# Kernel optimization log

Measured on AMD Instinct MI355X. Metric: run time of the kernel, lower is better.

Reference implementation:

```python
import jax, jax.numpy as jnp
import numpy as np

B = 4096
D = 64  # emb_dim, hardcoded in UserEmb/ItemEmb


def setup_inputs() -> dict:
    key = jax.random.key(0)
    ks = jax.random.split(key, 26)
    n = lambda k, shape, s=1.0: jax.random.normal(k, shape, dtype=jnp.float32) * s
    inp = {
        'user_emb': jax.random.randint(ks[0], (B, 4), 0, 6, dtype=jnp.int32),
        'item_emb': jax.random.randint(ks[1], (B, 10242), 0, 2, dtype=jnp.int32),
        'edge_emb': jnp.zeros((B,), dtype=jnp.int32),  # edges_emb has num_embeddings=1
        # UserEmb params
        'gender_tab': n(ks[2], (98, D)),
        'age_tab': n(ks[3], (7, D)),
        'occ_tab': n(ks[4], (21, D)),
        'area_tab': n(ks[5], (3402, D)),
        'user_W': n(ks[6], (4 * D, D), 0.05),  # stored [in,out]
        'user_b': n(ks[7], (D,), 0.05),
        # ItemEmb params
        'rate_tab': n(ks[8], (6, D)),
        'genre_W': n(ks[9], (25, D), 0.05),
        'director_W': n(ks[10], (2186, D), 0.02),
        'actor_W': n(ks[11], (8030, D), 0.01),
        'item_W': n(ks[12], (4 * D, D), 0.05),
        'item_b': n(ks[13], (D,), 0.05),
        # GLNFeat params (torch: randn * 0.5)
        'edges_tab': n(ks[14], (1, D)),
        'uu_w': n(ks[15], (D,), 0.5),
        'ui_w': n(ks[16], (D,), 0.5),
        'iu_w': n(ks[17], (D,), 0.5),
        'ii_w': n(ks[18], (D,), 0.5),
        'edge_W': n(ks[19], (D, D), 0.5),
        'uu_W1': n(ks[20], (D, D), 0.5),
        'ui_W1': n(ks[21], (D, D), 0.5),
        'iu_W1': n(ks[22], (D, D), 0.5),
        'ii_W1': n(ks[23], (D, D), 0.5),
    }
    return inp


def _lrelu(v):
    return jnp.where(v >= 0, v, 0.01 * v)  # nn.LeakyReLU default slope


def reference(user_emb, item_emb, edge_emb, gender_tab, age_tab, occ_tab, area_tab,
              user_W, user_b, rate_tab, genre_W, director_W, actor_W, item_W, item_b,
              edges_tab, uu_w, ui_w, iu_w, ii_w, edge_W, uu_W1, ui_W1, iu_W1, ii_W1):
    a = 0.12
    b = 0.12
    # UserEmb
    u_cat = jnp.concatenate([gender_tab[user_emb[:, 0]], age_tab[user_emb[:, 1]],
                             occ_tab[user_emb[:, 2]], area_tab[user_emb[:, 3]]], axis=1)
    x = (u_cat @ user_W + user_b) * a  # [B, D]
    # ItemEmb: multi-hot fields projected then mean-normalized by count
    genre = item_emb[:, 1:26].astype(jnp.float32)
    director = item_emb[:, 26:2212].astype(jnp.float32)
    actor = item_emb[:, 2212:10242].astype(jnp.float32)
    ge = (genre @ genre_W) / jnp.sum(genre, 1, keepdims=True)
    de = (director @ director_W) / jnp.sum(director, 1, keepdims=True)
    ae = (actor @ actor_W) / jnp.sum(actor, 1, keepdims=True)
    i_cat = jnp.concatenate([rate_tab[item_emb[:, 0]], ge, de, ae], axis=1)
    y = (i_cat @ item_W + item_b) * a  # [B, D]
    edge = edges_tab[edge_emb] * b  # [B, D]

    def outer_mm(u, v, M):
        # stop_gradient(outer(u, v) @ M) == u[:,None] * (v @ M), avoids [B,B]
        return jax.lax.stop_gradient(u[:, None] * (v @ M))

    xe = x * edge
    ye = y * edge
    x_xx = xe @ uu_w      # [B]
    x_xy_x = xe @ ui_w
    x_xy_y = ye @ ui_w
    t1 = outer_mm(x_xx, x_xx, x)
    t2 = outer_mm(x_xy_x, x_xy_y, y)
    x_buy = (_lrelu(t1 @ uu_W1) + _lrelu(t2 @ ui_W1)) / 2
    y_yy = ye @ ii_w
    y_yx_y = ye @ iu_w
    y_yx_x = xe @ iu_w
    t3 = outer_mm(y_yy, y_yy, y)
    t4 = outer_mm(y_yx_y, y_yx_x, x)
    y_buy = (_lrelu(t3 @ ii_W1) + _lrelu(t4 @ iu_W1)) / 2
    new = _lrelu(edge @ edge_W)
    return ((x_buy + x) / 2, (y_buy + y) / 2, (new + edge) / 2)
```

## Files before the change

kernel.cpp:

```cpp
#include <hip/hip_runtime.h>
#include <cstddef>

constexpr int BATCH = 4096;
constexpr int ITEM_COLS = 10242;

constexpr int R_GENDER = 0;
constexpr int R_AGE    = 98;
constexpr int R_OCC    = 105;
constexpr int R_AREA   = 126;
constexpr int R_RATE   = 3528;
constexpr int R_FU     = 3534;

__device__ const int CBASE[9]  = {0, 24, 1112, 2208, 3544, 4880, 6224, 7560, 8896};
__device__ const int VSTART[9] = {1, 26, 1119, 2212, 3550, 4888, 6227, 7565, 8903};
__device__ const int VEND[9]   = {26, 1119, 2212, 3550, 4888, 6227, 7565, 8903, 10242};
__device__ const int CUM[10]   = {0, 128, 1280, 2432, 3840, 5248, 6656, 8064, 9472, 10880};
constexpr int FB2COLS = 10880;
constexpr int NFUSEA = 884;
constexpr int NFUSET = FB2COLS / 64;

constexpr size_t OFF_FU  = 0;
constexpr size_t OFF_NEW = OFF_FU + (size_t)R_FU * 64;
constexpr size_t OFF_FBT = OFF_NEW + 64;
constexpr size_t OFF_X   = OFF_FBT + (size_t)64 * FB2COLS / 2;
constexpr size_t OFF_Y   = OFF_X + (size_t)BATCH * 64;
constexpr size_t OFF_P   = OFF_Y + (size_t)BATCH * 64;
constexpr size_t OFF_C   = OFF_P + 9ull * BATCH * 64;
constexpr size_t OFF_SP  = OFF_C + 9ull * BATCH;
constexpr size_t OFF_PB  = OFF_SP + 256ull * 256;
constexpr size_t OFF_SC  = OFF_PB + 4ull * 64;

typedef __attribute__((ext_vector_type(8))) short bf16x8;
typedef __attribute__((ext_vector_type(4))) float f32x4;

__device__ __forceinline__ float lrelu(float v) { return v >= 0.0f ? v : 0.01f * v; }

__device__ __forceinline__ unsigned bf_rne_pair(float lo, float hi) {
    unsigned ul = __builtin_bit_cast(unsigned, lo);
    unsigned uh = __builtin_bit_cast(unsigned, hi);
    ul += 0x7fffu + ((ul >> 16) & 1u);
    uh += 0x7fffu + ((uh >> 16) & 1u);
    return (ul >> 16) | (uh & 0xffff0000u);
}

__global__ __launch_bounds__(256) void k_fuse(
        const float* __restrict__ gender_tab, const float* __restrict__ age_tab,
        const float* __restrict__ occ_tab, const float* __restrict__ area_tab,
        const float* __restrict__ user_W, const float* __restrict__ rate_tab,
        const float* __restrict__ item_W, const float* __restrict__ edges_tab,
        const float* __restrict__ edge_W, const float* __restrict__ genre_W,
        const float* __restrict__ director_W, const float* __restrict__ actor_W,
        float* __restrict__ Fu, float* __restrict__ NEWt, short* __restrict__ Fbt2) {
    const int t = threadIdx.x;
    const int n = t & 63;
    const int rb = __builtin_amdgcn_readfirstlane(t >> 6);
    __shared__ float T[64 * 65];
    const int blk = blockIdx.x;

    if (blk < NFUSEA) {
        int r = blk * 4 + rb;
        if (r > R_FU) return;
        if (r == R_FU) {
            float acc = 0.0f;
#pragma unroll
            for (int k = 0; k < 64; ++k)
                acc = fmaf(edges_tab[k] * 0.12f, edge_W[k * 64 + n], acc);
            NEWt[n] = lrelu(acc);
            return;
        }
        const float* src;
        const float* W;
        if (r < R_AGE)       { src = gender_tab + (size_t)r * 64;            W = user_W;            }
        else if (r < R_OCC)  { src = age_tab    + (size_t)(r - R_AGE) * 64;  W = user_W + 64 * 64;  }
        else if (r < R_AREA) { src = occ_tab    + (size_t)(r - R_OCC) * 64;  W = user_W + 128 * 64; }
        else if (r < R_RATE) { src = area_tab   + (size_t)(r - R_AREA) * 64; W = user_W + 192 * 64; }
        else                 { src = rate_tab   + (size_t)(r - R_RATE) * 64; W = item_W;            }
        float acc = 0.0f;
#pragma unroll
        for (int k = 0; k < 64; ++k)
            acc = fmaf(src[k], W[k * 64 + n], acc);
        Fu[(size_t)r * 64 + n] = acc;
        return;
    }

    const int g0 = (blk - NFUSEA) * 64;
    int ch = 0;
    while (g0 >= CUM[ch + 1]) ++ch;
    const int kk0 = g0 - CUM[ch];
    const int lenp = CUM[ch + 1] - CUM[ch];
    const int cb = CBASE[ch], vs = VSTART[ch], ve = VEND[ch];

    for (int rl = 0; rl < 16; ++rl) {
        int r = rl * 4 + rb;
        int c = cb + kk0 + r;
        float acc = 0.0f;
        if (c >= vs && c < ve) {
            const float* src;
            const float* W;
            if (c < 26)        { src = genre_W    + (size_t)(c - 1) * 64;    W = item_W + 64 * 64;  }
            else if (c < 2212) { src = director_W + (size_t)(c - 26) * 64;   W = item_W + 128 * 64; }
            else               { src = actor_W    + (size_t)(c - 2212) * 64; W = item_W + 192 * 64; }
#pragma unroll
            for (int k = 0; k < 64; ++k)
                acc = fmaf(src[k], W[k * 64 + n], acc);
        }
        T[r * 65 + n] = acc;
    }
    __syncthreads();
    int n2 = t >> 2, sg = t & 3;
    unsigned dw[8];
#pragma unroll
    for (int d = 0; d < 8; ++d)
        dw[d] = bf_rne_pair(T[(sg * 16 + 2 * d) * 65 + n2], T[(sg * 16 + 2 * d + 1) * 65 + n2]);
    uint4* dst = (uint4*)(Fbt2 + (size_t)64 * CUM[ch] + (size_t)n2 * lenp + kk0 + sg * 16);
    dst[0] = make_uint4(dw[0], dw[1], dw[2], dw[3]);
    dst[1] = make_uint4(dw[4], dw[5], dw[6], dw[7]);
}

__global__ __launch_bounds__(256) void k_item(const int* __restrict__ item,
                                              const short* __restrict__ Fbt2,
                                              float* __restrict__ P, float* __restrict__ C) {
    const int ch = blockIdx.y;
    const int cb = CBASE[ch], vs = VSTART[ch], ve = VEND[ch];
    const int lo = vs - cb;
    const int hi = ve - cb;
    const int lenp = CUM[ch + 1] - CUM[ch];
    const short* FB = Fbt2 + (size_t)64 * CUM[ch];
    const int m0 = blockIdx.x * 64;
    const int t = threadIdx.x;
    const int lane = t & 63;
    const int w = __builtin_amdgcn_readfirstlane(t >> 6);
    const int q = lane >> 4, r16 = lane & 15;

    __shared__ short As[64 * 136];
    __shared__ short Bs[64 * 136];

    f32x4 acc[5];
#pragma unroll
    for (int s = 0; s < 5; ++s) acc[s] = (f32x4){0.f, 0.f, 0.f, 0.f};

    const short o = (r16 == 0) ? (short)0x3f80 : (short)0;
    const bf16x8 ones = {o, o, o, o, o, o, o, o};

    for (int kb = 0; kb < hi; kb += 128) {
        __syncthreads();
        const int c0 = cb + kb;
        if (c0 + 128 <= ITEM_COLS) {
#pragma unroll
            for (int it = 0; it < 16; ++it) {
                int f = it * 256 + t;
                int r = f >> 6, c2 = f & 63;
                int2 v = *(const int2*)(item + (size_t)(m0 + r) * ITEM_COLS + c0 + c2 * 2);
                unsigned d = (v.x ? 0x3f80u : 0u) | (v.y ? 0x3f800000u : 0u);
                *(unsigned*)(As + r * 136 + c2 * 2) = d;
            }
        } else {
#pragma unroll
            for (int it = 0; it < 32; ++it) {
                int f = it * 256 + t;
                int r = f >> 7, cc = f & 127;
                int c = c0 + cc;
                int v = (c < ITEM_COLS) ? item[(size_t)(m0 + r) * ITEM_COLS + c] : 0;
                As[r * 136 + cc] = v ? (short)0x3f80 : (short)0;
            }
        }
        {
            int nB = t >> 2, pt = t & 3;
            const short* fb = FB + (size_t)nB * lenp + kb;
#pragma unroll
            for (int p = 0; p < 4; ++p) {
                int off = (p * 4 + pt) * 8;
                *(uint4*)(Bs + nB * 136 + off) = *(const uint4*)(fb + off);
            }
        }
        __syncthreads();
        const bool edge = (kb < lo) || (kb + 128 > hi);
#pragma unroll
        for (int kt = 0; kt < 4; ++kt) {
            bf16x8 a = *(const bf16x8*)(As + (w * 16 + r16) * 136 + kt * 32 + q * 8);
            bf16x8 ov = ones;
            if (edge) {
#pragma unroll
                for (int j = 0; j < 8; ++j) {
                    int ks = kb + kt * 32 + q * 8 + j;
                    ov[j] = (ks >= lo && ks < hi) ? o : (short)0;
                }
            }
#pragma unroll
            for (int s = 0; s < 4; ++s) {
                bf16x8 b = *(const bf16x8*)(Bs + (s * 16 + r16) * 136 + kt * 32 + q * 8);
                acc[s] = __builtin_amdgcn_mfma_f32_16x16x32_bf16(a, b, acc[s], 0, 0, 0);
            }
            acc[4] = __builtin_amdgcn_mfma_f32_16x16x32_bf16(a, ov, acc[4], 0, 0, 0);
        }
    }
    const size_t pb = (size_t)ch * BATCH + m0 + w * 16 + q * 4;
#pragma unroll
    for (int reg = 0; reg < 4; ++reg) {
        float* pr = P + (pb + reg) * 64 + r16;
        pr[0] = acc[0][reg];
        pr[16] = acc[1][reg];
        pr[32] = acc[2][reg];
        pr[48] = acc[3][reg];
    }
    if (r16 == 0) {
#pragma unroll
        for (int reg = 0; reg < 4; ++reg)
            C[(size_t)ch * BATCH + m0 + w * 16 + q * 4 + reg] = acc[4][reg];
    }
}

__device__ __forceinline__ float wred(float v) {
#pragma unroll
    for (int m = 1; m < 64; m <<= 1) v += __shfl_xor(v, m, 64);
    return v;
}

__global__ __launch_bounds__(256) void k_mid(const int* __restrict__ item, const int* __restrict__ edge_emb,
                                             const int* __restrict__ user_emb,
                                             const float* __restrict__ Fu, const float* __restrict__ user_b,
                                             const float* __restrict__ P, const float* __restrict__ C,
                                             const float* __restrict__ item_b, const float* __restrict__ edges_tab,
                                             const float* __restrict__ uu_w, const float* __restrict__ ui_w,
                                             const float* __restrict__ iu_w, const float* __restrict__ ii_w,
                                             float* __restrict__ X, float* __restrict__ Y,
                                             float* __restrict__ SC, float* __restrict__ SP) {
    const int t = threadIdx.x;
    const int n = t & 63;
    const int wv = __builtin_amdgcn_readfirstlane(t >> 6);
    const float uuw = uu_w[n], uiw = ui_w[n], iuw = iu_w[n], iiw = ii_w[n];
    const float ib = item_b[n], ub = user_b[n];
    const size_t cs = (size_t)BATCH * 64;
    float s1 = 0.0f, s2 = 0.0f, s3 = 0.0f, s4 = 0.0f;

    for (int i = 0; i < 4; ++i) {
        int b = blockIdx.x * 16 + wv * 4 + i;
        const int* ue = user_emb + (size_t)b * 4;
        float x = (Fu[(size_t)(R_GENDER + ue[0]) * 64 + n]
                 + Fu[(size_t)(R_AGE    + ue[1]) * 64 + n]
                 + Fu[(size_t)(R_OCC    + ue[2]) * 64 + n]
                 + Fu[(size_t)(R_AREA   + ue[3]) * 64 + n] + ub) * 0.12f;
        X[(size_t)b * 64 + n] = x;
        int ri = item[(size_t)b * ITEM_COLS];
        size_t base = (size_t)b * 64 + n;
        float sg = P[base];
        float sd = P[base + cs] + P[base + 2 * cs];
        float sa = P[base + 3 * cs] + P[base + 4 * cs] + P[base + 5 * cs]
                 + P[base + 6 * cs] + P[base + 7 * cs] + P[base + 8 * cs];
        float cg = C[b];
        float cd = C[BATCH + b] + C[2 * BATCH + b];
        float ca = C[3 * BATCH + b] + C[4 * BATCH + b] + C[5 * BATCH + b]
                 + C[6 * BATCH + b] + C[7 * BATCH + b] + C[8 * BATCH + b];
        float y = (Fu[(size_t)(R_RATE + ri) * 64 + n] + sg / cg + sd / cd + sa / ca + ib) * 0.12f;
        Y[(size_t)b * 64 + n] = y;
        float e = edges_tab[(size_t)edge_emb[b] * 64 + n] * 0.12f;
        float xe = x * e, ye = y * e;
        float r1 = wred(xe * uuw);
        float r2 = wred(xe * uiw);
        float r3 = wred(xe * iuw);
        float r4 = wred(ye * uiw);
        float r5 = wred(ye * iiw);
        float r6 = wred(ye * iuw);
        if (n == 0) {
            SC[b] = r1; SC[BATCH + b] = r2; SC[2 * BATCH + b] = r5; SC[3 * BATCH + b] = r6;
        }
        s1 = fmaf(r1, x, s1);
        s2 = fmaf(r4, y, s2);
        s3 = fmaf(r5, y, s3);
        s4 = fmaf(r3, x, s4);
    }
    __shared__ float sp[4][4][64];
    sp[wv][0][n] = s1; sp[wv][1][n] = s2; sp[wv][2][n] = s3; sp[wv][3][n] = s4;
    __syncthreads();
    int i2 = t >> 6;
    float v = sp[0][i2][n] + sp[1][i2][n] + sp[2][i2][n] + sp[3][i2][n];
    SP[(size_t)blockIdx.x * 256 + t] = v;
}

__global__ __launch_bounds__(1024) void k_red(const float* __restrict__ SP,
                                              const float* __restrict__ uu_W1, const float* __restrict__ ui_W1,
                                              const float* __restrict__ iu_W1, const float* __restrict__ ii_W1,
                                              float* __restrict__ PB) {
    int t = threadIdx.x;
    int sub = t >> 8, i = (t >> 6) & 3, n = t & 63;
    float s = 0.0f;
    for (int wb = sub * 64; wb < sub * 64 + 64; ++wb)
        s += SP[(size_t)wb * 256 + i * 64 + n];
    __shared__ float red[4][4][64];
    red[sub][i][n] = s;
    __syncthreads();
    float sv = red[0][i][n] + red[1][i][n] + red[2][i][n] + red[3][i][n];
    __shared__ float sl[4][64];
    if (t < 256) sl[i][n] = sv;
    __syncthreads();
    if (t < 256) {
        const float* W1 = (i == 0) ? uu_W1 : (i == 1) ? ui_W1 : (i == 2) ? ii_W1 : iu_W1;
        float p = 0.0f;
#pragma unroll
        for (int k = 0; k < 64; ++k) p = fmaf(sl[i][k], W1[k * 64 + n], p);
        PB[i * 64 + n] = p;
    }
}

__global__ __launch_bounds__(256) void k_out(const float* __restrict__ X, const float* __restrict__ Y,
                                             const float* __restrict__ SC, const float* __restrict__ PB,
                                             const float* __restrict__ NEWt, const float* __restrict__ edges_tab,
                                             const int* __restrict__ edge_emb, float* __restrict__ out) {
    int t = threadIdx.x;
    int b = blockIdx.x * 4 + (t >> 6);
    int n = t & 63;
    float xx = SC[b], xyx = SC[BATCH + b], yy = SC[2 * BATCH + b], yxy = SC[3 * BATCH + b];
    float p1 = PB[n], p2 = PB[64 + n], p3 = PB[128 + n], p4 = PB[192 + n];
    float x = X[(size_t)b * 64 + n], y = Y[(size_t)b * 64 + n];
    float o1 = ((lrelu(xx * p1) + lrelu(xyx * p2)) * 0.5f + x) * 0.5f;
    float o2 = ((lrelu(yy * p3) + lrelu(yxy * p4)) * 0.5f + y) * 0.5f;
    int ei = edge_emb[b];
    float e = edges_tab[(size_t)ei * 64 + n] * 0.12f;
    float o3 = (NEWt[n] + e) * 0.5f;
    out[(size_t)b * 64 + n] = o1;
    out[((size_t)BATCH + b) * 64 + n] = o2;
    out[((size_t)2 * BATCH + b) * 64 + n] = o3;
}

extern "C" void kernel_launch(void* const* d_in, const int* in_sizes, int n_in,
                              void* d_out, int out_size, void* d_ws, size_t ws_size,
                              hipStream_t stream) {
    (void)in_sizes; (void)n_in; (void)out_size; (void)ws_size;
    const int*   user_emb   = (const int*)  d_in[0];
    const int*   item_emb   = (const int*)  d_in[1];
    const int*   edge_emb   = (const int*)  d_in[2];
    const float* gender_tab = (const float*)d_in[3];
    const float* age_tab    = (const float*)d_in[4];
    const float* occ_tab    = (const float*)d_in[5];
    const float* area_tab   = (const float*)d_in[6];
    const float* user_W     = (const float*)d_in[7];
    const float* user_b     = (const float*)d_in[8];
    const float* rate_tab   = (const float*)d_in[9];
    const float* genre_W    = (const float*)d_in[10];
    const float* director_W = (const float*)d_in[11];
    const float* actor_W    = (const float*)d_in[12];
    const float* item_W     = (const float*)d_in[13];
    const float* item_b     = (const float*)d_in[14];
    const float* edges_tab  = (const float*)d_in[15];
    const float* uu_w       = (const float*)d_in[16];
    const float* ui_w       = (const float*)d_in[17];
    const float* iu_w       = (const float*)d_in[18];
    const float* ii_w       = (const float*)d_in[19];
    const float* edge_W     = (const float*)d_in[20];
    const float* uu_W1      = (const float*)d_in[21];
    const float* ui_W1      = (const float*)d_in[22];
    const float* iu_W1      = (const float*)d_in[23];
    const float* ii_W1      = (const float*)d_in[24];

    float* ws   = (float*)d_ws;
    float* Fu   = ws + OFF_FU;
    float* NEWt = ws + OFF_NEW;
    short* Fbt2 = (short*)(ws + OFF_FBT);
    float* X    = ws + OFF_X;
    float* Y    = ws + OFF_Y;
    float* P    = ws + OFF_P;
    float* C    = ws + OFF_C;
    float* SP   = ws + OFF_SP;
    float* PB   = ws + OFF_PB;
    float* SC   = ws + OFF_SC;
    float* out  = (float*)d_out;

    hipLaunchKernelGGL(k_fuse, dim3(NFUSEA + NFUSET), dim3(256), 0, stream,
                       gender_tab, age_tab, occ_tab, area_tab, user_W, rate_tab,
                       item_W, edges_tab, edge_W, genre_W, director_W, actor_W,
                       Fu, NEWt, Fbt2);
    hipLaunchKernelGGL(k_item, dim3(BATCH / 64, 9), dim3(256), 0, stream, item_emb, Fbt2, P, C);
    hipLaunchKernelGGL(k_mid, dim3(BATCH / 16), dim3(256), 0, stream,
                       item_emb, edge_emb, user_emb, Fu, user_b, P, C, item_b, edges_tab,
                       uu_w, ui_w, iu_w, ii_w, X, Y, SC, SP);
    hipLaunchKernelGGL(k_red, dim3(1), dim3(1024), 0, stream, SP, uu_W1, ui_W1, iu_W1, ii_W1, PB);
    hipLaunchKernelGGL(k_out, dim3(BATCH / 4), dim3(256), 0, stream,
                       X, Y, SC, PB, NEWt, edges_tab, edge_emb, out);
}
```

Baseline: 348.8 us.

## Balance item GEMM k-slices, prefetch tiles into registers, fuse reduction into output

The item multi-hot GEMM is repartitioned from 9 uneven channel blocks into 15 balanced k-slices over a flat k-tile index. Each k-tile's A and B data is prefetched into registers while the current tile is consumed, with hand-placed barriers replacing __syncthreads. This aims to fix load imbalance and hide global load latency. The single-block k_red kernel is folded into k_out, so every output block redundantly reduces SP and computes the W1 projections. That removes one launch but adds duplicated reduction work per block.

```diff
diff --git a/kernel.cpp b/kernel.cpp
--- a/kernel.cpp
+++ b/kernel.cpp
@@ -11,11 +11,24 @@
 constexpr int R_RATE   = 3528;
 constexpr int R_FU     = 3534;
 
-__device__ const int CBASE[9]  = {0, 24, 1112, 2208, 3544, 4880, 6224, 7560, 8896};
-__device__ const int VSTART[9] = {1, 26, 1119, 2212, 3550, 4888, 6227, 7565, 8903};
-__device__ const int VEND[9]   = {26, 1119, 2212, 3550, 4888, 6227, 7565, 8903, 10242};
-__device__ const int CUM[10]   = {0, 128, 1280, 2432, 3840, 5248, 6656, 8064, 9472, 10880};
+__device__ const int CUM[10] = {0, 128, 1280, 2432, 3840, 5248, 6656, 8064, 9472, 10880};
+__device__ const int DLT[9]  = {0, -104, -168, -224, -296, -368, -432, -504, -576};
+__device__ const int LOG[9]  = {1, 130, 1287, 2436, 3846, 5256, 6659, 8069, 9479};
+__device__ const int HIG[9]  = {26, 1223, 2380, 3774, 5184, 6595, 7997, 9407, 10818};
 constexpr int FB2COLS = 10880;
+constexpr int NSLICE  = 15;
+__device__ const int TS_[16] = {0, 1, 7, 13, 19, 25, 31, 37, 43, 49, 55, 61, 67, 73, 79, 85};
+__device__ const int TCH[85] = {
+    0,
+    1,1,1,1,1,1,1,1,1,
+    2,2,2,2,2,2,2,2,2,
+    3,3,3,3,3,3,3,3,3,3,3,
+    4,4,4,4,4,4,4,4,4,4,4,
+    5,5,5,5,5,5,5,5,5,5,5,
+    6,6,6,6,6,6,6,6,6,6,6,
+    7,7,7,7,7,7,7,7,7,7,7,
+    8,8,8,8,8,8,8,8,8,8,8};
+
 constexpr int NFUSEA = 884;
 constexpr int NFUSET = FB2COLS / 64;
 
@@ -25,10 +38,9 @@
 constexpr size_t OFF_X   = OFF_FBT + (size_t)64 * FB2COLS / 2;
 constexpr size_t OFF_Y   = OFF_X + (size_t)BATCH * 64;
 constexpr size_t OFF_P   = OFF_Y + (size_t)BATCH * 64;
-constexpr size_t OFF_C   = OFF_P + 9ull * BATCH * 64;
-constexpr size_t OFF_SP  = OFF_C + 9ull * BATCH;
-constexpr size_t OFF_PB  = OFF_SP + 256ull * 256;
-constexpr size_t OFF_SC  = OFF_PB + 4ull * 64;
+constexpr size_t OFF_C   = OFF_P + (size_t)NSLICE * BATCH * 64;
+constexpr size_t OFF_SP  = OFF_C + (size_t)NSLICE * BATCH;
+constexpr size_t OFF_SC  = OFF_SP + 256ull * 256;
 
 typedef __attribute__((ext_vector_type(8))) short bf16x8;
 typedef __attribute__((ext_vector_type(4))) float f32x4;
@@ -86,15 +98,14 @@
     const int g0 = (blk - NFUSEA) * 64;
     int ch = 0;
     while (g0 >= CUM[ch + 1]) ++ch;
-    const int kk0 = g0 - CUM[ch];
-    const int lenp = CUM[ch + 1] - CUM[ch];
-    const int cb = CBASE[ch], vs = VSTART[ch], ve = VEND[ch];
+    const int lo = LOG[ch], hi = HIG[ch], dl = DLT[ch];
 
     for (int rl = 0; rl < 16; ++rl) {
         int r = rl * 4 + rb;
-        int c = cb + kk0 + r;
+        int g = g0 + r;
         float acc = 0.0f;
-        if (c >= vs && c < ve) {
+        if (g >= lo && g < hi) {
+            int c = g + dl;
             const float* src;
             const float* W;
             if (c < 26)        { src = genre_W    + (size_t)(c - 1) * 64;    W = item_W + 64 * 64;  }
@@ -112,7 +123,7 @@
 #pragma unroll
     for (int d = 0; d < 8; ++d)
         dw[d] = bf_rne_pair(T[(sg * 16 + 2 * d) * 65 + n2], T[(sg * 16 + 2 * d + 1) * 65 + n2]);
-    uint4* dst = (uint4*)(Fbt2 + (size_t)64 * CUM[ch] + (size_t)n2 * lenp + kk0 + sg * 16);
+    uint4* dst = (uint4*)(Fbt2 + (size_t)n2 * FB2COLS + g0 + sg * 16);
     dst[0] = make_uint4(dw[0], dw[1], dw[2], dw[3]);
     dst[1] = make_uint4(dw[4], dw[5], dw[6], dw[7]);
 }
@@ -120,12 +131,8 @@
 __global__ __launch_bounds__(256) void k_item(const int* __restrict__ item,
                                               const short* __restrict__ Fbt2,
                                               float* __restrict__ P, float* __restrict__ C) {
-    const int ch = blockIdx.y;
-    const int cb = CBASE[ch], vs = VSTART[ch], ve = VEND[ch];
-    const int lo = vs - cb;
-    const int hi = ve - cb;
-    const int lenp = CUM[ch + 1] - CUM[ch];
-    const short* FB = Fbt2 + (size_t)64 * CUM[ch];
+    const int slc = blockIdx.y;
+    const int kt0 = TS_[slc], kt1 = TS_[slc + 1];
     const int m0 = blockIdx.x * 64;
     const int t = threadIdx.x;
     const int lane = t & 63;
@@ -142,59 +149,75 @@
     const short o = (r16 == 0) ? (short)0x3f80 : (short)0;
     const bf16x8 ones = {o, o, o, o, o, o, o, o};
 
-    for (int kb = 0; kb < hi; kb += 128) {
-        __syncthreads();
-        const int c0 = cb + kb;
+    int2 av[16];
+    uint4 bv[4];
+    const int nB = t >> 2, pt = t & 3;
+    const int* arow = item + (size_t)(m0 + w) * ITEM_COLS + 2 * lane;
+    const short* brow = Fbt2 + (size_t)nB * FB2COLS;
+
+    auto fetch = [&](int kt) {
+        const int ch = TCH[kt];
+        const int c0 = kt * 128 + DLT[ch];
         if (c0 + 128 <= ITEM_COLS) {
+            const int* ap = arow + c0;
+#pragma unroll
+            for (int it = 0; it < 16; ++it)
+                av[it] = *(const int2*)(ap + (size_t)it * 4 * ITEM_COLS);
+        } else {
+            const bool ok = (c0 + 2 * lane) <= (ITEM_COLS - 2);
+            const int ccl = ok ? (c0 + 2 * lane) : (ITEM_COLS - 2);
+            const int* ap = item + (size_t)(m0 + w) * ITEM_COLS + ccl;
 #pragma unroll
             for (int it = 0; it < 16; ++it) {
-                int f = it * 256 + t;
-                int r = f >> 6, c2 = f & 63;
-                int2 v = *(const int2*)(item + (size_t)(m0 + r) * ITEM_COLS + c0 + c2 * 2);
-                unsigned d = (v.x ? 0x3f80u : 0u) | (v.y ? 0x3f800000u : 0u);
-                *(unsigned*)(As + r * 136 + c2 * 2) = d;
+                int2 v = *(const int2*)(ap + (size_t)it * 4 * ITEM_COLS);
+                av[it].x = ok ? v.x : 0;
+                av[it].y = ok ? v.y : 0;
             }
-        } else {
-#pragma unroll
-            for (int it = 0; it < 32; ++it) {
-                int f = it * 256 + t;
-                int r = f >> 7, cc = f & 127;
-                int c = c0 + cc;
-                int v = (c < ITEM_COLS) ? item[(size_t)(m0 + r) * ITEM_COLS + c] : 0;
-                As[r * 136 + cc] = v ? (short)0x3f80 : (short)0;
-            }
-        }
-        {
-            int nB = t >> 2, pt = t & 3;
-            const short* fb = FB + (size_t)nB * lenp + kb;
-#pragma unroll
-            for (int p = 0; p < 4; ++p) {
-                int off = (p * 4 + pt) * 8;
-                *(uint4*)(Bs + nB * 136 + off) = *(const uint4*)(fb + off);
-            }
-        }
-        __syncthreads();
-        const bool edge = (kb < lo) || (kb + 128 > hi);
-#pragma unroll
-        for (int kt = 0; kt < 4; ++kt) {
-            bf16x8 a = *(const bf16x8*)(As + (w * 16 + r16) * 136 + kt * 32 + q * 8);
+        }
+        const short* bp = brow + kt * 128;
+#pragma unroll
+        for (int p = 0; p < 4; ++p)
+            bv[p] = *(const uint4*)(bp + (p * 4 + pt) * 8);
+    };
+
+    fetch(kt0);
+    for (int kt = kt0; kt < kt1; ++kt) {
+#pragma unroll
+        for (int it = 0; it < 16; ++it) {
+            unsigned d = (av[it].x ? 0x3f80u : 0u) | (av[it].y ? 0x3f800000u : 0u);
+            *(unsigned*)(As + (it * 4 + w) * 136 + 2 * lane) = d;
+        }
+#pragma unroll
+        for (int p = 0; p < 4; ++p)
+            *(uint4*)(Bs + nB * 136 + (p * 4 + pt) * 8) = bv[p];
+        if (kt + 1 < kt1) fetch(kt + 1);
+        asm volatile("s_waitcnt lgkmcnt(0)\n\ts_barrier" ::: "memory");
+
+        const int ch = TCH[kt];
+        const int g0 = kt * 128;
+        const int lo = LOG[ch] - g0, hi = HIG[ch] - g0;
+        const bool edge = (lo > 0) || (hi < 128);
+#pragma unroll
+        for (int ks = 0; ks < 4; ++ks) {
+            bf16x8 a = *(const bf16x8*)(As + (w * 16 + r16) * 136 + ks * 32 + q * 8);
             bf16x8 ov = ones;
             if (edge) {
 #pragma unroll
                 for (int j = 0; j < 8; ++j) {
-                    int ks = kb + kt * 32 + q * 8 + j;
-                    ov[j] = (ks >= lo && ks < hi) ? o : (short)0;
+                    int kk = ks * 32 + q * 8 + j;
+                    ov[j] = (kk >= lo && kk < hi) ? o : (short)0;
                 }
             }
 #pragma unroll
             for (int s = 0; s < 4; ++s) {
-                bf16x8 b = *(const bf16x8*)(Bs + (s * 16 + r16) * 136 + kt * 32 + q * 8);
+                bf16x8 b = *(const bf16x8*)(Bs + (s * 16 + r16) * 136 + ks * 32 + q * 8);
                 acc[s] = __builtin_amdgcn_mfma_f32_16x16x32_bf16(a, b, acc[s], 0, 0, 0);
             }
             acc[4] = __builtin_amdgcn_mfma_f32_16x16x32_bf16(a, ov, acc[4], 0, 0, 0);
         }
-    }
-    const size_t pb = (size_t)ch * BATCH + m0 + w * 16 + q * 4;
+        asm volatile("s_barrier" ::: "memory");
+    }
+    const size_t pb = (size_t)slc * BATCH + m0 + w * 16 + q * 4;
 #pragma unroll
     for (int reg = 0; reg < 4; ++reg) {
         float* pr = P + (pb + reg) * 64 + r16;
@@ -206,7 +229,7 @@
     if (r16 == 0) {
 #pragma unroll
         for (int reg = 0; reg < 4; ++reg)
-            C[(size_t)ch * BATCH + m0 + w * 16 + q * 4 + reg] = acc[4][reg];
+            C[(size_t)slc * BATCH + m0 + w * 16 + q * 4 + reg] = acc[4][reg];
     }
 }
 
@@ -244,13 +267,12 @@
         int ri = item[(size_t)b * ITEM_COLS];
         size_t base = (size_t)b * 64 + n;
         float sg = P[base];
-        float sd = P[base + cs] + P[base + 2 * cs];
-        float sa = P[base + 3 * cs] + P[base + 4 * cs] + P[base + 5 * cs]
-                 + P[base + 6 * cs] + P[base + 7 * cs] + P[base + 8 * cs];
         float cg = C[b];
-        float cd = C[BATCH + b] + C[2 * BATCH + b];
-        float ca = C[3 * BATCH + b] + C[4 * BATCH + b] + C[5 * BATCH + b]
-                 + C[6 * BATCH + b] + C[7 * BATCH + b] + C[8 * BATCH + b];
+        float sd = 0.0f, cd = 0.0f, sa = 0.0f, ca = 0.0f;
+#pragma unroll
+        for (int s5 = 1; s5 < 4; ++s5) { sd += P[base + s5 * cs]; cd += C[s5 * BATCH + b]; }
+#pragma unroll
+        for (int s5 = 4; s5 < NSLICE; ++s5) { sa += P[base + s5 * cs]; ca += C[s5 * BATCH + b]; }
         float y = (Fu[(size_t)(R_RATE + ri) * 64 + n] + sg / cg + sd / cd + sa / ca + ib) * 0.12f;
         Y[(size_t)b * 64 + n] = y;
         float e = edges_tab[(size_t)edge_emb[b] * 64 + n] * 0.12f;
@@ -277,49 +299,42 @@
     SP[(size_t)blockIdx.x * 256 + t] = v;
 }
 
-__global__ __launch_bounds__(1024) void k_red(const float* __restrict__ SP,
-                                              const float* __restrict__ uu_W1, const float* __restrict__ ui_W1,
-                                              const float* __restrict__ iu_W1, const float* __restrict__ ii_W1,
-                                              float* __restrict__ PB) {
-    int t = threadIdx.x;
-    int sub = t >> 8, i = (t >> 6) & 3, n = t & 63;
+__global__ __launch_bounds__(256) void k_out(const float* __restrict__ X, const float* __restrict__ Y,
+                                             const float* __restrict__ SC, const float* __restrict__ SP,
+                                             const float* __restrict__ NEWt, const float* __restrict__ edges_tab,
+                                             const int* __restrict__ edge_emb,
+                                             const float* __restrict__ uu_W1, const float* __restrict__ ui_W1,
+                                             const float* __restrict__ iu_W1, const float* __restrict__ ii_W1,
+                                             float* __restrict__ out) {
+    const int t = threadIdx.x;
+    const int i = t >> 6, n = t & 63;
     float s = 0.0f;
-    for (int wb = sub * 64; wb < sub * 64 + 64; ++wb)
-        s += SP[(size_t)wb * 256 + i * 64 + n];
-    __shared__ float red[4][4][64];
-    red[sub][i][n] = s;
+    for (int wb = 0; wb < 256; ++wb) s += SP[(size_t)wb * 256 + t];
+    __shared__ float sl2[4][64];
+    sl2[i][n] = s;
     __syncthreads();
-    float sv = red[0][i][n] + red[1][i][n] + red[2][i][n] + red[3][i][n];
-    __shared__ float sl[4][64];
-    if (t < 256) sl[i][n] = sv;
+    const float* W1 = (i == 0) ? uu_W1 : (i == 1) ? ui_W1 : (i == 2) ? ii_W1 : iu_W1;
+    float p = 0.0f;
+#pragma unroll
+    for (int k = 0; k < 64; ++k) p = fmaf(sl2[i][k], W1[k * 64 + n], p);
+    __shared__ float pbs[4][64];
+    pbs[i][n] = p;
     __syncthreads();
-    if (t < 256) {
-        const float* W1 = (i == 0) ? uu_W1 : (i == 1) ? ui_W1 : (i == 2) ? ii_W1 : iu_W1;
-        float p = 0.0f;
-#pragma unroll
-        for (int k = 0; k < 64; ++k) p = fmaf(sl[i][k], W1[k * 64 + n], p);
-        PB[i * 64 + n] = p;
-    }
-}
-
-__global__ __launch_bounds__(256) void k_out(const float* __restrict__ X, const float* __restrict__ Y,
-                                             const float* __restrict__ SC, const float* __restrict__ PB,
-                                             const float* __restrict__ NEWt, const float* __restrict__ edges_tab,
-                                             const int* __restrict__ edge_emb, float* __restrict__ out) {
-    int t = threadIdx.x;
-    int b = blockIdx.x * 4 + (t >> 6);
-    int n = t & 63;
-    float xx = SC[b], xyx = SC[BATCH + b], yy = SC[2 * BATCH + b], yxy = SC[3 * BATCH + b];
-    float p1 = PB[n], p2 = PB[64 + n], p3 = PB[128 + n], p4 = PB[192 + n];
-    float x = X[(size_t)b * 64 + n], y = Y[(size_t)b * 64 + n];
-    float o1 = ((lrelu(xx * p1) + lrelu(xyx * p2)) * 0.5f + x) * 0.5f;
-    float o2 = ((lrelu(yy * p3) + lrelu(yxy * p4)) * 0.5f + y) * 0.5f;
-    int ei = edge_emb[b];
-    float e = edges_tab[(size_t)ei * 64 + n] * 0.12f;
-    float o3 = (NEWt[n] + e) * 0.5f;
-    out[(size_t)b * 64 + n] = o1;
-    out[((size_t)BATCH + b) * 64 + n] = o2;
-    out[((size_t)2 * BATCH + b) * 64 + n] = o3;
+    const float p1 = pbs[0][n], p2 = pbs[1][n], p3 = pbs[2][n], p4 = pbs[3][n];
+    const float nw = NEWt[n];
+#pragma unroll
+    for (int j = 0; j < 8; ++j) {
+        int b = blockIdx.x * 32 + j * 4 + i;
+        float xx = SC[b], xyx = SC[BATCH + b], yy = SC[2 * BATCH + b], yxy = SC[3 * BATCH + b];
+        float x = X[(size_t)b * 64 + n], y = Y[(size_t)b * 64 + n];
+        float o1 = ((lrelu(xx * p1) + lrelu(xyx * p2)) * 0.5f + x) * 0.5f;
+        float o2 = ((lrelu(yy * p3) + lrelu(yxy * p4)) * 0.5f + y) * 0.5f;
+        float e = edges_tab[(size_t)edge_emb[b] * 64 + n] * 0.12f;
+        float o3 = (nw + e) * 0.5f;
+        out[(size_t)b * 64 + n] = o1;
+        out[((size_t)BATCH + b) * 64 + n] = o2;
+        out[((size_t)2 * BATCH + b) * 64 + n] = o3;
+    }
 }
 
 extern "C" void kernel_launch(void* const* d_in, const int* in_sizes, int n_in,
@@ -361,7 +376,6 @@
     float* P    = ws + OFF_P;
     float* C    = ws + OFF_C;
     float* SP   = ws + OFF_SP;
-    float* PB   = ws + OFF_PB;
     float* SC   = ws + OFF_SC;
     float* out  = (float*)d_out;
 
@@ -369,11 +383,11 @@
                        gender_tab, age_tab, occ_tab, area_tab, user_W, rate_tab,
                        item_W, edges_tab, edge_W, genre_W, director_W, actor_W,
                        Fu, NEWt, Fbt2);
-    hipLaunchKernelGGL(k_item, dim3(BATCH / 64, 9), dim3(256), 0, stream, item_emb, Fbt2, P, C);
+    hipLaunchKernelGGL(k_item, dim3(BATCH / 64, NSLICE), dim3(256), 0, stream, item_emb, Fbt2, P, C);
     hipLaunchKernelGGL(k_mid, dim3(BATCH / 16), dim3(256), 0, stream,
                        item_emb, edge_emb, user_emb, Fu, user_b, P, C, item_b, edges_tab,
                        uu_w, ui_w, iu_w, ii_w, X, Y, SC, SP);
-    hipLaunchKernelGGL(k_red, dim3(1), dim3(1024), 0, stream, SP, uu_W1, ui_W1, iu_W1, ii_W1, PB);
-    hipLaunchKernelGGL(k_out, dim3(BATCH / 4), dim3(256), 0, stream,
-                       X, Y, SC, PB, NEWt, edges_tab, edge_emb, out);
-}
+    hipLaunchKernelGGL(k_out, dim3(BATCH / 32), dim3(256), 0, stream,
+                       X, Y, SC, SP, NEWt, edges_tab, edge_emb,
+                       uu_W1, ui_W1, iu_W1, ii_W1, out);
+}
```

Result: slower. 366.1 us (+5.0%).
